# Performance work log

Hardware: AMD Instinct MI355X
Metric: run time of the kernel (lower is better)

The kernel has to match this reference:

```python
import jax, jax.numpy as jnp
import numpy as np

NUM_KNOTS = 64   # max(num_knots, degree+5)
DEGREE = 3
N_ROWS = 1048576

def make_knots():
    inner = np.linspace(0.0, 1.0, NUM_KNOTS - 2 * DEGREE)
    knots = np.concatenate([np.zeros(DEGREE), inner, np.ones(DEGREE)])
    return jnp.asarray(knots, dtype=jnp.float32)

def setup_inputs() -> dict:
    key = jax.random.key(0)
    x = jax.random.normal(key, (N_ROWS, 1), dtype=jnp.float32)
    return {"x": x, "knots": make_knots()}

def cox_de_boor(x, t, degree):
    # x: [N] in [0,1), t: [K] non-decreasing knots. Returns [N, K-degree-1].
    K = t.shape[0]
    # degree-0: indicator of half-open knot intervals (empty for repeated knots)
    B = ((x[:, None] >= t[None, :-1]) & (x[:, None] < t[None, 1:])).astype(x.dtype)  # [N, K-1]
    for d in range(1, degree + 1):
        m = K - 1 - d  # number of basis functions at this degree
        ld = t[d:d + m] - t[:m]            # left denominators
        rd = t[d + 1:d + 1 + m] - t[1:1 + m]  # right denominators
        left = jnp.where(ld > 0, (x[:, None] - t[None, :m]) / jnp.where(ld > 0, ld, 1.0), 0.0)
        right = jnp.where(rd > 0, (t[None, d + 1:d + 1 + m] - x[:, None]) / jnp.where(rd > 0, rd, 1.0), 0.0)
        B = left * B[:, :m] + right * B[:, 1:m + 1]
    return B  # [N, K-degree-1]

def reference(x, knots):
    xf = x.reshape(-1)
    x_min = jnp.min(xf)
    x_max = jnp.max(xf)
    # matches torch: (x - min) / (max - min + 1e-8); result strictly in [0, 1)
    xn = (xf - x_min) / (x_max - x_min + 1e-8)
    return cox_de_boor(xn, knots, DEGREE)  # [N, 60]
```

## Files before the change

kernel.cpp:

```cpp
#include <hip/hip_runtime.h>


#define N_BASIS 60

__device__ __forceinline__ float fast_rcp(float a) {
    return __builtin_amdgcn_rcpf(a);
}

__global__ __launch_bounds__(256) void k_partial_minmax(
    const float* __restrict__ x, float* __restrict__ ws, int n4) {
    const int tid = threadIdx.x;
    int gid = blockIdx.x * 256 + tid;
    const int stride = gridDim.x * 256;
    const float4* __restrict__ x4 = (const float4*)x;

    float mn = 3.4028235e38f, mx = -3.4028235e38f;
    for (int i = gid; i < n4; i += stride) {
        float4 v = x4[i];
        mn = fminf(mn, fminf(fminf(v.x, v.y), fminf(v.z, v.w)));
        mx = fmaxf(mx, fmaxf(fmaxf(v.x, v.y), fmaxf(v.z, v.w)));
    }
#pragma unroll
    for (int off = 32; off > 0; off >>= 1) {
        mn = fminf(mn, __shfl_down(mn, off, 64));
        mx = fmaxf(mx, __shfl_down(mx, off, 64));
    }
    __shared__ float smn[4], smx[4];
    if ((tid & 63) == 0) { smn[tid >> 6] = mn; smx[tid >> 6] = mx; }
    __syncthreads();
    if (tid == 0) {
        mn = fminf(fminf(smn[0], smn[1]), fminf(smn[2], smn[3]));
        mx = fmaxf(fmaxf(smx[0], smx[1]), fmaxf(smx[2], smx[3]));
        ws[blockIdx.x] = mn;
        ws[256 + blockIdx.x] = mx;
    }
}

__global__ __launch_bounds__(256) void k_final_minmax(float* __restrict__ ws) {
    const int tid = threadIdx.x;
    float mn = ws[tid];
    float mx = ws[256 + tid];
#pragma unroll
    for (int off = 32; off > 0; off >>= 1) {
        mn = fminf(mn, __shfl_down(mn, off, 64));
        mx = fmaxf(mx, __shfl_down(mx, off, 64));
    }
    __shared__ float smn[4], smx[4];
    if ((tid & 63) == 0) { smn[tid >> 6] = mn; smx[tid >> 6] = mx; }
    __syncthreads();
    if (tid == 0) {
        mn = fminf(fminf(smn[0], smn[1]), fminf(smn[2], smn[3]));
        mx = fmaxf(fmaxf(smx[0], smx[1]), fmaxf(smx[2], smx[3]));
        ws[512] = mn;
        ws[513] = (mx - mn) + 1e-8f;
    }
}

__global__ __launch_bounds__(256) void k_bspline(
    const float* __restrict__ x, const float* __restrict__ knots,
    const float* __restrict__ ws, float* __restrict__ out, int nrows) {
    __shared__ float t[64];
    if (threadIdx.x < 64) t[threadIdx.x] = knots[threadIdx.x];
    __syncthreads();

    const int row = blockIdx.x * 256 + threadIdx.x;
    if (row >= nrows) return;

    const float xmin = ws[512];
    const float range = ws[513];
    const float xn = (x[row] - xmin) / range;

    const bool live = (xn < 1.0f) && (xn >= 0.0f);

    int ii = (int)(xn * 57.0f);
    ii = ii < 0 ? 0 : (ii > 56 ? 56 : ii);
    int i = ii + 3;
    if (xn < t[i]) i -= 1;
    else if (xn >= t[i + 1]) i += 1;
    i = i < 3 ? 3 : (i > 59 ? 59 : i);

    const float l1 = xn - t[i];
    const float l2 = xn - t[i - 1];
    const float l3 = xn - t[i - 2];
    const float r1 = t[i + 1] - xn;
    const float r2 = t[i + 2] - xn;
    const float r3 = t[i + 3] - xn;

    float N0 = 1.0f, N1, N2, N3, temp, saved;
    temp = N0 * fast_rcp(r1 + l1);
    N0 = r1 * temp;
    N1 = l1 * temp;
    temp = N0 * fast_rcp(r1 + l2);
    N0 = r1 * temp;
    saved = l2 * temp;
    temp = N1 * fast_rcp(r2 + l1);
    N1 = saved + r2 * temp;
    N2 = l1 * temp;
    temp = N0 * fast_rcp(r1 + l3);
    N0 = r1 * temp;
    saved = l3 * temp;
    temp = N1 * fast_rcp(r2 + l2);
    N1 = saved + r2 * temp;
    saved = l2 * temp;
    temp = N2 * fast_rcp(r3 + l1);
    N2 = saved + r3 * temp;
    N3 = l1 * temp;

    const float g = live ? 1.0f : 0.0f;
    N0 *= g; N1 *= g; N2 *= g; N3 *= g;

    const int base = i - 3;
    const int m = base & 3;
    const int qa = base >> 2;
    const int qb = qa + 1;

    float4 QA, QB;
    QA.x = (m == 0) ? N0 : 0.0f;
    QA.y = (m == 0) ? N1 : ((m == 1) ? N0 : 0.0f);
    QA.z = (m == 0) ? N2 : ((m == 1) ? N1 : ((m == 2) ? N0 : 0.0f));
    QA.w = (m == 0) ? N3 : ((m == 1) ? N2 : ((m == 2) ? N1 : N0));
    QB.x = (m == 1) ? N3 : ((m == 2) ? N2 : ((m == 3) ? N1 : 0.0f));
    QB.y = (m == 2) ? N3 : ((m == 3) ? N2 : 0.0f);
    QB.z = (m == 3) ? N3 : 0.0f;
    QB.w = 0.0f;

    float4* __restrict__ orow = (float4*)(out + (size_t)row * N_BASIS);
#pragma unroll
    for (int q = 0; q < 15; ++q) {
        float4 v;
        const bool a = (q == qa), b = (q == qb);
        v.x = a ? QA.x : (b ? QB.x : 0.0f);
        v.y = a ? QA.y : (b ? QB.y : 0.0f);
        v.z = a ? QA.z : (b ? QB.z : 0.0f);
        v.w = a ? QA.w : 0.0f;
        orow[q] = v;
    }
}

extern "C" void kernel_launch(void* const* d_in, const int* in_sizes, int n_in,
                              void* d_out, int out_size, void* d_ws, size_t ws_size,
                              hipStream_t stream) {
    const float* x = (const float*)d_in[0];
    const float* knots = (const float*)d_in[1];
    float* out = (float*)d_out;
    float* ws = (float*)d_ws;
    const int nrows = in_sizes[0];

    k_partial_minmax<<<256, 256, 0, stream>>>(x, ws, nrows / 4);
    k_final_minmax<<<1, 256, 0, stream>>>(ws);
    k_bspline<<<(nrows + 255) / 256, 256, 0, stream>>>(x, knots, ws, out, nrows);
}
```

Baseline: 274.3 us.

## Stage basis values in LDS and write output rows with coalesced float4 stores

Each thread now writes its four nonzero basis values and span index to shared memory. The block then stores its 256x60 output tile cooperatively, with consecutive threads writing consecutive float4s. Before, each thread wrote its own 240-byte row, so a wavefront's stores were strided. The change adds a block barrier, LDS traffic and an integer divide by 15, and it drops the row bounds check, so N must be a multiple of 256.

```diff
diff --git a/kernel.cpp b/kernel.cpp
--- a/kernel.cpp
+++ b/kernel.cpp
@@ -58,14 +58,16 @@
 
 __global__ __launch_bounds__(256) void k_bspline(
     const float* __restrict__ x, const float* __restrict__ knots,
-    const float* __restrict__ ws, float* __restrict__ out, int nrows) {
+    const float* __restrict__ ws, float* __restrict__ out) {
     __shared__ float t[64];
-    if (threadIdx.x < 64) t[threadIdx.x] = knots[threadIdx.x];
+    __shared__ float4 sN[256];
+    __shared__ int sBase[256];
+
+    const int tid = threadIdx.x;
+    if (tid < 64) t[tid] = knots[tid];
     __syncthreads();
 
-    const int row = blockIdx.x * 256 + threadIdx.x;
-    if (row >= nrows) return;
-
+    const int row = blockIdx.x * 256 + tid;
     const float xmin = ws[512];
     const float range = ws[513];
     const float xn = (x[row] - xmin) / range;
@@ -107,33 +109,30 @@
     N3 = l1 * temp;
 
     const float g = live ? 1.0f : 0.0f;
-    N0 *= g; N1 *= g; N2 *= g; N3 *= g;
+    float4 Nv;
+    Nv.x = N0 * g; Nv.y = N1 * g; Nv.z = N2 * g; Nv.w = N3 * g;
+    sN[tid] = Nv;
+    sBase[tid] = i - 3;
+    __syncthreads();
 
-    const int base = i - 3;
-    const int m = base & 3;
-    const int qa = base >> 2;
-    const int qb = qa + 1;
-
-    float4 QA, QB;
-    QA.x = (m == 0) ? N0 : 0.0f;
-    QA.y = (m == 0) ? N1 : ((m == 1) ? N0 : 0.0f);
-    QA.z = (m == 0) ? N2 : ((m == 1) ? N1 : ((m == 2) ? N0 : 0.0f));
-    QA.w = (m == 0) ? N3 : ((m == 1) ? N2 : ((m == 2) ? N1 : N0));
-    QB.x = (m == 1) ? N3 : ((m == 2) ? N2 : ((m == 3) ? N1 : 0.0f));
-    QB.y = (m == 2) ? N3 : ((m == 3) ? N2 : 0.0f);
-    QB.z = (m == 3) ? N3 : 0.0f;
-    QB.w = 0.0f;
-
-    float4* __restrict__ orow = (float4*)(out + (size_t)row * N_BASIS);
+    float4* __restrict__ o4 = (float4*)out + (size_t)blockIdx.x * 3840;
 #pragma unroll
-    for (int q = 0; q < 15; ++q) {
+    for (int it = 0; it < 15; ++it) {
+        const int p = tid + it * 256;
+        const unsigned r = (unsigned)p / 15u;
+        const int j = p - (int)r * 15;
+        const float4 N = sN[r];
+        const int b = sBase[r];
+        const int d0 = (j << 2) - b;
         float4 v;
-        const bool a = (q == qa), b = (q == qb);
-        v.x = a ? QA.x : (b ? QB.x : 0.0f);
-        v.y = a ? QA.y : (b ? QB.y : 0.0f);
-        v.z = a ? QA.z : (b ? QB.z : 0.0f);
-        v.w = a ? QA.w : 0.0f;
-        orow[q] = v;
+        v.x = (d0 == 0) ? N.x : (d0 == 1) ? N.y : (d0 == 2) ? N.z : (d0 == 3) ? N.w : 0.0f;
+        const int d1 = d0 + 1;
+        v.y = (d1 == 0) ? N.x : (d1 == 1) ? N.y : (d1 == 2) ? N.z : (d1 == 3) ? N.w : 0.0f;
+        const int d2 = d0 + 2;
+        v.z = (d2 == 0) ? N.x : (d2 == 1) ? N.y : (d2 == 2) ? N.z : (d2 == 3) ? N.w : 0.0f;
+        const int d3 = d0 + 3;
+        v.w = (d3 == 0) ? N.x : (d3 == 1) ? N.y : (d3 == 2) ? N.z : (d3 == 3) ? N.w : 0.0f;
+        o4[p] = v;
     }
 }
 
@@ -148,5 +147,5 @@
 
     k_partial_minmax<<<256, 256, 0, stream>>>(x, ws, nrows / 4);
     k_final_minmax<<<1, 256, 0, stream>>>(ws);
-    k_bspline<<<(nrows + 255) / 256, 256, 0, stream>>>(x, knots, ws, out, nrows);
+    k_bspline<<<nrows / 256, 256, 0, stream>>>(x, knots, ws, out);
 }
```

New measurement: 251.3 us. 8.4% less time.
